# Kernel tuning notes

Hardware: AMD Instinct MI355X
Metric: run time of the kernel (lower is better)

The kernel has to match this reference:

```python
import jax, jax.numpy as jnp
import numpy as np

N_NODES = 100000
N_EDGES = 1600000
F_IN = 128
F_OUT = 32


def setup_inputs() -> dict:
    key = jax.random.key(0)
    k1, k2, k3 = jax.random.split(key, 3)
    x = jax.random.normal(k1, (N_NODES, F_IN), dtype=jnp.float32)
    edge_index = jax.random.randint(k2, (2, N_EDGES), 0, N_NODES, dtype=jnp.int64)
    # Glorot-style init for the GCNConv linear weight [F_IN, F_OUT]
    W = jax.random.normal(k3, (F_IN, F_OUT), dtype=jnp.float32) * (1.0 / np.sqrt(F_IN))
    b = jnp.zeros((F_OUT,), dtype=jnp.float32)
    return {"x": x, "edge_index": edge_index, "W": W, "b": b}


def reference(x, edge_index, W, b):
    N = x.shape[0]
    # --- add self loops (PyG GCNConv default) ---
    loops = jnp.arange(N, dtype=edge_index.dtype)
    src = jnp.concatenate([edge_index[0], loops])  # message sources j
    dst = jnp.concatenate([edge_index[1], loops])  # aggregation targets i
    # --- symmetric normalization: deg^-1/2[src] * deg^-1/2[dst] ---
    ones = jnp.ones(src.shape[0], dtype=x.dtype)
    deg = jax.ops.segment_sum(ones, dst, num_segments=N)  # in-degree incl. self loop
    dinv = jnp.where(deg > 0, jax.lax.rsqrt(deg), jnp.zeros_like(deg))
    norm = dinv[src] * dinv[dst]  # [E+N]
    # --- linear transform then gather-scale-scatter aggregate ---
    h = x @ W  # [N, F_OUT]
    msgs = h[src] * norm[:, None]  # [E+N, F_OUT]
    out = jax.ops.segment_sum(msgs, dst, num_segments=N)  # [N, F_OUT]
    return out + b
```

## Files before the change

kernel.cpp:

```cpp
#include <hip/hip_runtime.h>
#include <hip/hip_fp16.h>

#define N_NODES 100000
#define N_EDGES 1600000
#define F_IN    128
#define F_OUT   32

#define BKT_SHIFT  7
#define BKT_SIZE   128
#define NBKT       782
#define BKT_STRIDE 2560
#define BIN_TILE   4096
#define EPT        16
#define NTILES     ((N_EDGES + BIN_TILE - 1) / BIN_TILE)

#define AGG_SPLIT  4
#define SUB        32
#define SUB_STRIDE 768

typedef _Float16 f16x8 __attribute__((ext_vector_type(8)));
typedef float    f32x4 __attribute__((ext_vector_type(4)));

__global__ void init_kernel(int* __restrict__ gcur) {
    int i = blockIdx.x * blockDim.x + threadIdx.x;
    if (i < NBKT) gcur[i] = 0;
}

__global__ __launch_bounds__(256) void bin_kernel(const int* __restrict__ ei,
                                                  int* __restrict__ gcur,
                                                  unsigned int* __restrict__ binned) {
    __shared__ int cnt[NBKT], pos[NBKT], gbase[NBKT];
    int t = threadIdx.x;
    for (int b = t; b < NBKT; b += 256) { cnt[b] = 0; pos[b] = 0; }
    __syncthreads();
    int ebase = blockIdx.x * BIN_TILE;
    unsigned int pk[EPT];
    short bkt[EPT];
#pragma unroll
    for (int k = 0; k < EPT; ++k) {
        int e = ebase + k * 256 + t;
        if (e < N_EDGES) {
            int s = ei[e];
            int d = ei[N_EDGES + e];
            bkt[k] = (short)(d >> BKT_SHIFT);
            pk[k]  = (unsigned)s | ((unsigned)(d & (BKT_SIZE - 1)) << 25);
            atomicAdd(&cnt[bkt[k]], 1);
        } else {
            bkt[k] = -1;
        }
    }
    __syncthreads();
    for (int b = t; b < NBKT; b += 256)
        if (cnt[b] > 0) gbase[b] = atomicAdd(&gcur[b], cnt[b]);
    __syncthreads();
#pragma unroll
    for (int k = 0; k < EPT; ++k) {
        if (bkt[k] >= 0) {
            int r = atomicAdd(&pos[bkt[k]], 1);
            int p = gbase[bkt[k]] + r;
            if (p < BKT_STRIDE)
                binned[(size_t)bkt[k] * BKT_STRIDE + p] = pk[k];
        }
    }
}

__global__ __launch_bounds__(256) void dinv_from_bins_kernel(const unsigned int* __restrict__ binned,
                                                             const int* __restrict__ gcur,
                                                             float* __restrict__ dinv) {
    __shared__ int cnt[BKT_SIZE];
    int t = threadIdx.x;
    int b = blockIdx.x;
    if (t < BKT_SIZE) cnt[t] = 0;
    __syncthreads();
    int ne = gcur[b];
    if (ne > BKT_STRIDE) ne = BKT_STRIDE;
    const unsigned int* eb = binned + (size_t)b * BKT_STRIDE;
    for (int i = t; i < ne; i += 256)
        atomicAdd(&cnt[eb[i] >> 25], 1);
    __syncthreads();
    int gnode = b * BKT_SIZE + t;
    if (t < BKT_SIZE && gnode < N_NODES)
        dinv[gnode] = rsqrtf((float)(cnt[t] + 1));
}

#define WH_STRIDE 136
__global__ __launch_bounds__(256) void matmul_kernel(const float4* __restrict__ x4,
                                                     const float* __restrict__ W,
                                                     const float* __restrict__ dinv,
                                                     __half* __restrict__ hs) {
    __shared__ _Float16 Wh[F_OUT * WH_STRIDE];
    int t = threadIdx.x;
    {
        int col = t & 31, kb = (t >> 5) * 16;
        for (int u = 0; u < 16; ++u)
            Wh[col * WH_STRIDE + kb + u] = (_Float16)W[(kb + u) * F_OUT + col];
    }
    __syncthreads();

    int w = t >> 6, l = t & 63;
    int lr = l & 15, kg = l >> 4;
    int row = blockIdx.x * 64 + w * 16 + lr;
    const float4* xr = x4 + (size_t)row * 32;
    bool rok = row < N_NODES;

    f16x8 a[4];
#pragma unroll
    for (int ks = 0; ks < 4; ++ks) {
        float4 v0, v1;
        if (rok) {
            v0 = xr[ks * 8 + kg * 2];
            v1 = xr[ks * 8 + kg * 2 + 1];
        } else {
            v0 = make_float4(0, 0, 0, 0);
            v1 = v0;
        }
        f16x8 av;
        av[0] = (_Float16)v0.x; av[1] = (_Float16)v0.y;
        av[2] = (_Float16)v0.z; av[3] = (_Float16)v0.w;
        av[4] = (_Float16)v1.x; av[5] = (_Float16)v1.y;
        av[6] = (_Float16)v1.z; av[7] = (_Float16)v1.w;
        a[ks] = av;
    }

    f32x4 c0 = {0.f, 0.f, 0.f, 0.f}, c1 = {0.f, 0.f, 0.f, 0.f};
#pragma unroll
    for (int ks = 0; ks < 4; ++ks) {
        f16x8 b0 = *(const f16x8*)&Wh[lr * WH_STRIDE + ks * 32 + kg * 8];
        f16x8 b1 = *(const f16x8*)&Wh[(16 + lr) * WH_STRIDE + ks * 32 + kg * 8];
        c0 = __builtin_amdgcn_mfma_f32_16x16x32_f16(a[ks], b0, c0, 0, 0, 0);
        c1 = __builtin_amdgcn_mfma_f32_16x16x32_f16(a[ks], b1, c1, 0, 0, 0);
    }

    int orow0 = blockIdx.x * 64 + w * 16 + kg * 4;
#pragma unroll
    for (int i = 0; i < 4; ++i) {
        int orow = orow0 + i;
        if (orow < N_NODES) {
            float dv = dinv[orow];
            hs[(size_t)orow * F_OUT + lr]      = (__half)(c0[i] * dv);
            hs[(size_t)orow * F_OUT + 16 + lr] = (__half)(c1[i] * dv);
        }
    }
}

__device__ inline void acc4(uint2 u, float& a0, float& a1, float& a2, float& a3) {
    float2 f0 = __half22float2(*(__half2*)&u.x);
    float2 f1 = __half22float2(*(__half2*)&u.y);
    a0 += f0.x; a1 += f0.y; a2 += f1.x; a3 += f1.y;
}

__global__ __launch_bounds__(256) void aggregate_kernel(const unsigned int* __restrict__ binned,
                                                        const int* __restrict__ gcur,
                                                        const uint2* __restrict__ hs4,
                                                        const float* __restrict__ dinv,
                                                        const float* __restrict__ bias,
                                                        float* __restrict__ out) {
    __shared__ int scan[SUB];
    __shared__ int rp[SUB + 1];
    __shared__ int cur[SUB];
    __shared__ int se[SUB_STRIDE];
    int t = threadIdx.x;
    int b   = blockIdx.x >> 2;
    int sub = blockIdx.x & 3;
    int ne = gcur[b];
    if (ne > BKT_STRIDE) ne = BKT_STRIDE;
    const unsigned int* eb = binned + (size_t)b * BKT_STRIDE;

    if (t < SUB) scan[t] = 0;
    __syncthreads();

    unsigned pk[10];
#pragma unroll
    for (int k = 0; k < 10; ++k) {
        int i = t + k * 256;
        pk[k] = (i < ne) ? eb[i] : 0xFFFFFFFFu;
    }
#pragma unroll
    for (int k = 0; k < 10; ++k) {
        if (pk[k] != 0xFFFFFFFFu) {
            int dl = (int)(pk[k] >> 25);
            if ((dl >> 5) == sub) atomicAdd(&scan[dl & 31], 1);
        }
    }
    __syncthreads();
    int v = (t < SUB) ? scan[t] : 0;
    for (int off = 1; off < SUB; off <<= 1) {
        int add = (t < SUB && t >= off) ? scan[t - off] : 0;
        __syncthreads();
        if (t < SUB) scan[t] += add;
        __syncthreads();
    }
    if (t < SUB) {
        int ex = scan[t] - v;
        if (ex > SUB_STRIDE) ex = SUB_STRIDE;
        rp[t] = ex;
        cur[t] = ex;
    }
    if (t == 0) rp[SUB] = (scan[SUB - 1] < SUB_STRIDE) ? 0 : SUB_STRIDE;
    __syncthreads();
    if (t == 0) {
        int tot = scan[SUB - 1];
        rp[SUB] = (tot > SUB_STRIDE) ? SUB_STRIDE : tot;
    }
    __syncthreads();
#pragma unroll
    for (int k = 0; k < 10; ++k) {
        if (pk[k] != 0xFFFFFFFFu) {
            int dl = (int)(pk[k] >> 25);
            if ((dl >> 5) == sub) {
                int r = atomicAdd(&cur[dl & 31], 1);
                if (r < SUB_STRIDE) se[r] = (int)(pk[k] & 0x1FFFFFF);
            }
        }
    }
    __syncthreads();

    int n = t >> 3, j4 = t & 7;
    int gnode = b * BKT_SIZE + sub * SUB + n;
    if (gnode >= N_NODES) return;
    float4 bv = *(const float4*)&bias[j4 * 4];
    int beg = rp[n], end = rp[n + 1];
    float a0 = 0.f, a1 = 0.f, a2 = 0.f, a3 = 0.f;
    int p = beg;
    for (; p + 7 < end; p += 8) {
        uint2 u0 = hs4[(size_t)se[p]     * 8 + j4];
        uint2 u1 = hs4[(size_t)se[p + 1] * 8 + j4];
        uint2 u2 = hs4[(size_t)se[p + 2] * 8 + j4];
        uint2 u3 = hs4[(size_t)se[p + 3] * 8 + j4];
        uint2 u4 = hs4[(size_t)se[p + 4] * 8 + j4];
        uint2 u5 = hs4[(size_t)se[p + 5] * 8 + j4];
        uint2 u6 = hs4[(size_t)se[p + 6] * 8 + j4];
        uint2 u7 = hs4[(size_t)se[p + 7] * 8 + j4];
        acc4(u0, a0, a1, a2, a3); acc4(u1, a0, a1, a2, a3);
        acc4(u2, a0, a1, a2, a3); acc4(u3, a0, a1, a2, a3);
        acc4(u4, a0, a1, a2, a3); acc4(u5, a0, a1, a2, a3);
        acc4(u6, a0, a1, a2, a3); acc4(u7, a0, a1, a2, a3);
    }
    for (; p + 3 < end; p += 4) {
        uint2 u0 = hs4[(size_t)se[p]     * 8 + j4];
        uint2 u1 = hs4[(size_t)se[p + 1] * 8 + j4];
        uint2 u2 = hs4[(size_t)se[p + 2] * 8 + j4];
        uint2 u3 = hs4[(size_t)se[p + 3] * 8 + j4];
        acc4(u0, a0, a1, a2, a3); acc4(u1, a0, a1, a2, a3);
        acc4(u2, a0, a1, a2, a3); acc4(u3, a0, a1, a2, a3);
    }
    for (; p < end; ++p) {
        uint2 u0 = hs4[(size_t)se[p] * 8 + j4];
        acc4(u0, a0, a1, a2, a3);
    }
    float dv = dinv[gnode];
    uint2 us = hs4[(size_t)gnode * 8 + j4];
    float2 s0 = __half22float2(*(__half2*)&us.x);
    float2 s1 = __half22float2(*(__half2*)&us.y);
    float4 o;
    o.x = bv.x + dv * (a0 + s0.x);
    o.y = bv.y + dv * (a1 + s0.y);
    o.z = bv.z + dv * (a2 + s1.x);
    o.w = bv.w + dv * (a3 + s1.y);
    *(float4*)&out[(size_t)gnode * F_OUT + j4 * 4] = o;
}

extern "C" void kernel_launch(void* const* d_in, const int* in_sizes, int n_in,
                              void* d_out, int out_size, void* d_ws, size_t ws_size,
                              hipStream_t stream) {
    const float* x  = (const float*)d_in[0];
    const int*   ei = (const int*)d_in[1];
    const float* W  = (const float*)d_in[2];
    const float* b  = (const float*)d_in[3];
    float* out = (float*)d_out;

    int*          gcur   = (int*)d_ws;
    unsigned int* binned = (unsigned int*)(gcur + 1024);
    float*        dinv   = (float*)(binned + (size_t)NBKT * BKT_STRIDE);
    __half*       hs     = (__half*)(dinv + ((N_NODES + 3) & ~3));

    const int B = 256;

    init_kernel<<<1, 1024, 0, stream>>>(gcur);

    bin_kernel<<<NTILES, B, 0, stream>>>(ei, gcur, binned);

    dinv_from_bins_kernel<<<NBKT, B, 0, stream>>>(binned, gcur, dinv);

    matmul_kernel<<<(N_NODES + 63) / 64, B, 0, stream>>>((const float4*)x, W, dinv, hs);

    aggregate_kernel<<<NBKT * AGG_SPLIT, B, 0, stream>>>(binned, gcur, (const uint2*)hs, dinv, b, out);
}
```

Measured before the change: 75.13 us.

## Fuse degree computation into matmul and reuse atomic ranks in binning

Removes the separate dinv kernel. Each matmul block now covers one 128-node bucket, counts that bucket's in-degrees in shared memory and applies the normalization locally. The aggregate kernel computes dinv from its own per-node counts instead of reading a global array. Both bin and aggregate kernels keep the rank returned by the first shared atomic, which drops the second atomic pass. Binning uses 512-thread blocks with larger tiles. The cost is an extra pass over the binned edges inside matmul and larger blocks, which may lower occupancy.

```diff
diff --git a/kernel.cpp b/kernel.cpp
--- a/kernel.cpp
+++ b/kernel.cpp
@@ -10,9 +10,11 @@
 #define BKT_SIZE   128
 #define NBKT       782
 #define BKT_STRIDE 2560
-#define BIN_TILE   4096
-#define EPT        16
-#define NTILES     ((N_EDGES + BIN_TILE - 1) / BIN_TILE)
+
+#define BIN_THREADS 512
+#define BIN_TILE    8192
+#define EPT         (BIN_TILE / BIN_THREADS)
+#define NTILES      ((N_EDGES + BIN_TILE - 1) / BIN_TILE)
 
 #define AGG_SPLIT  4
 #define SUB        32
@@ -26,80 +28,76 @@
     if (i < NBKT) gcur[i] = 0;
 }
 
-__global__ __launch_bounds__(256) void bin_kernel(const int* __restrict__ ei,
-                                                  int* __restrict__ gcur,
-                                                  unsigned int* __restrict__ binned) {
-    __shared__ int cnt[NBKT], pos[NBKT], gbase[NBKT];
+__global__ __launch_bounds__(BIN_THREADS) void bin_kernel(const int* __restrict__ ei,
+                                                          int* __restrict__ gcur,
+                                                          unsigned int* __restrict__ binned) {
+    __shared__ int cnt[NBKT], gbase[NBKT];
     int t = threadIdx.x;
-    for (int b = t; b < NBKT; b += 256) { cnt[b] = 0; pos[b] = 0; }
+    for (int b = t; b < NBKT; b += BIN_THREADS) cnt[b] = 0;
     __syncthreads();
     int ebase = blockIdx.x * BIN_TILE;
     unsigned int pk[EPT];
+    int rk[EPT];
     short bkt[EPT];
 #pragma unroll
     for (int k = 0; k < EPT; ++k) {
-        int e = ebase + k * 256 + t;
+        int e = ebase + k * BIN_THREADS + t;
         if (e < N_EDGES) {
             int s = ei[e];
             int d = ei[N_EDGES + e];
             bkt[k] = (short)(d >> BKT_SHIFT);
             pk[k]  = (unsigned)s | ((unsigned)(d & (BKT_SIZE - 1)) << 25);
-            atomicAdd(&cnt[bkt[k]], 1);
+            rk[k]  = atomicAdd(&cnt[bkt[k]], 1);
         } else {
             bkt[k] = -1;
         }
     }
     __syncthreads();
-    for (int b = t; b < NBKT; b += 256)
+    for (int b = t; b < NBKT; b += BIN_THREADS)
         if (cnt[b] > 0) gbase[b] = atomicAdd(&gcur[b], cnt[b]);
     __syncthreads();
 #pragma unroll
     for (int k = 0; k < EPT; ++k) {
         if (bkt[k] >= 0) {
-            int r = atomicAdd(&pos[bkt[k]], 1);
-            int p = gbase[bkt[k]] + r;
+            int p = gbase[bkt[k]] + rk[k];
             if (p < BKT_STRIDE)
                 binned[(size_t)bkt[k] * BKT_STRIDE + p] = pk[k];
         }
     }
 }
 
-__global__ __launch_bounds__(256) void dinv_from_bins_kernel(const unsigned int* __restrict__ binned,
-                                                             const int* __restrict__ gcur,
-                                                             float* __restrict__ dinv) {
-    __shared__ int cnt[BKT_SIZE];
+#define WH_STRIDE 136
+__global__ __launch_bounds__(512) void matmul_kernel(const float4* __restrict__ x4,
+                                                     const float* __restrict__ W,
+                                                     const unsigned int* __restrict__ binned,
+                                                     const int* __restrict__ gcur,
+                                                     __half* __restrict__ hs) {
+    __shared__ _Float16 Wh[F_OUT * WH_STRIDE];
+    __shared__ int cnt128[BKT_SIZE];
+    __shared__ float dinvL[BKT_SIZE];
     int t = threadIdx.x;
     int b = blockIdx.x;
-    if (t < BKT_SIZE) cnt[t] = 0;
-    __syncthreads();
+
+    if (t < BKT_SIZE) cnt128[t] = 0;
+    {
+        int col = t & 31, kb = (t >> 5) * 8;
+        for (int u = 0; u < 8; ++u)
+            Wh[col * WH_STRIDE + kb + u] = (_Float16)W[(kb + u) * F_OUT + col];
+    }
+    __syncthreads();
+
     int ne = gcur[b];
     if (ne > BKT_STRIDE) ne = BKT_STRIDE;
     const unsigned int* eb = binned + (size_t)b * BKT_STRIDE;
-    for (int i = t; i < ne; i += 256)
-        atomicAdd(&cnt[eb[i] >> 25], 1);
-    __syncthreads();
-    int gnode = b * BKT_SIZE + t;
-    if (t < BKT_SIZE && gnode < N_NODES)
-        dinv[gnode] = rsqrtf((float)(cnt[t] + 1));
-}
-
-#define WH_STRIDE 136
-__global__ __launch_bounds__(256) void matmul_kernel(const float4* __restrict__ x4,
-                                                     const float* __restrict__ W,
-                                                     const float* __restrict__ dinv,
-                                                     __half* __restrict__ hs) {
-    __shared__ _Float16 Wh[F_OUT * WH_STRIDE];
-    int t = threadIdx.x;
-    {
-        int col = t & 31, kb = (t >> 5) * 16;
-        for (int u = 0; u < 16; ++u)
-            Wh[col * WH_STRIDE + kb + u] = (_Float16)W[(kb + u) * F_OUT + col];
-    }
+    for (int i = t; i < ne; i += 512)
+        atomicAdd(&cnt128[eb[i] >> 25], 1);
+    __syncthreads();
+    if (t < BKT_SIZE) dinvL[t] = rsqrtf((float)(cnt128[t] + 1));
     __syncthreads();
 
     int w = t >> 6, l = t & 63;
     int lr = l & 15, kg = l >> 4;
-    int row = blockIdx.x * 64 + w * 16 + lr;
+    int row = b * 128 + w * 16 + lr;
     const float4* xr = x4 + (size_t)row * 32;
     bool rok = row < N_NODES;
 
@@ -131,12 +129,12 @@
         c1 = __builtin_amdgcn_mfma_f32_16x16x32_f16(a[ks], b1, c1, 0, 0, 0);
     }
 
-    int orow0 = blockIdx.x * 64 + w * 16 + kg * 4;
+    int lrow0 = w * 16 + kg * 4;
 #pragma unroll
     for (int i = 0; i < 4; ++i) {
-        int orow = orow0 + i;
+        int orow = b * 128 + lrow0 + i;
         if (orow < N_NODES) {
-            float dv = dinv[orow];
+            float dv = dinvL[lrow0 + i];
             hs[(size_t)orow * F_OUT + lr]      = (__half)(c0[i] * dv);
             hs[(size_t)orow * F_OUT + 16 + lr] = (__half)(c1[i] * dv);
         }
@@ -152,12 +150,11 @@
 __global__ __launch_bounds__(256) void aggregate_kernel(const unsigned int* __restrict__ binned,
                                                         const int* __restrict__ gcur,
                                                         const uint2* __restrict__ hs4,
-                                                        const float* __restrict__ dinv,
                                                         const float* __restrict__ bias,
                                                         float* __restrict__ out) {
-    __shared__ int scan[SUB];
+    __shared__ int cnt[SUB];
+    __shared__ int sc[SUB];
     __shared__ int rp[SUB + 1];
-    __shared__ int cur[SUB];
     __shared__ int se[SUB_STRIDE];
     int t = threadIdx.x;
     int b   = blockIdx.x >> 2;
@@ -166,10 +163,11 @@
     if (ne > BKT_STRIDE) ne = BKT_STRIDE;
     const unsigned int* eb = binned + (size_t)b * BKT_STRIDE;
 
-    if (t < SUB) scan[t] = 0;
+    if (t < SUB) cnt[t] = 0;
     __syncthreads();
 
     unsigned pk[10];
+    int rk[10];
 #pragma unroll
     for (int k = 0; k < 10; ++k) {
         int i = t + k * 256;
@@ -177,40 +175,39 @@
     }
 #pragma unroll
     for (int k = 0; k < 10; ++k) {
+        rk[k] = -1;
         if (pk[k] != 0xFFFFFFFFu) {
             int dl = (int)(pk[k] >> 25);
-            if ((dl >> 5) == sub) atomicAdd(&scan[dl & 31], 1);
-        }
-    }
-    __syncthreads();
-    int v = (t < SUB) ? scan[t] : 0;
+            if ((dl >> 5) == sub) rk[k] = atomicAdd(&cnt[dl & 31], 1);
+        }
+    }
+    __syncthreads();
+    int v = (t < SUB) ? cnt[t] : 0;
+    if (t < SUB) sc[t] = v;
+    __syncthreads();
     for (int off = 1; off < SUB; off <<= 1) {
-        int add = (t < SUB && t >= off) ? scan[t - off] : 0;
+        int add = (t < SUB && t >= off) ? sc[t - off] : 0;
         __syncthreads();
-        if (t < SUB) scan[t] += add;
+        if (t < SUB) sc[t] += add;
         __syncthreads();
     }
     if (t < SUB) {
-        int ex = scan[t] - v;
-        if (ex > SUB_STRIDE) ex = SUB_STRIDE;
-        rp[t] = ex;
-        cur[t] = ex;
-    }
-    if (t == 0) rp[SUB] = (scan[SUB - 1] < SUB_STRIDE) ? 0 : SUB_STRIDE;
+        int ex = sc[t] - v;
+        rp[t] = (ex < SUB_STRIDE) ? ex : SUB_STRIDE;
+    }
+    if (t == 0) rp[SUB] = 0;
     __syncthreads();
     if (t == 0) {
-        int tot = scan[SUB - 1];
+        int tot = sc[SUB - 1];
         rp[SUB] = (tot > SUB_STRIDE) ? SUB_STRIDE : tot;
     }
     __syncthreads();
 #pragma unroll
     for (int k = 0; k < 10; ++k) {
-        if (pk[k] != 0xFFFFFFFFu) {
+        if (rk[k] >= 0) {
             int dl = (int)(pk[k] >> 25);
-            if ((dl >> 5) == sub) {
-                int r = atomicAdd(&cur[dl & 31], 1);
-                if (r < SUB_STRIDE) se[r] = (int)(pk[k] & 0x1FFFFFF);
-            }
+            int pos = rp[dl & 31] + rk[k];
+            if (pos < SUB_STRIDE) se[pos] = (int)(pk[k] & 0x1FFFFFF);
         }
     }
     __syncthreads();
@@ -219,7 +216,10 @@
     int gnode = b * BKT_SIZE + sub * SUB + n;
     if (gnode >= N_NODES) return;
     float4 bv = *(const float4*)&bias[j4 * 4];
-    int beg = rp[n], end = rp[n + 1];
+    int deg = cnt[n];
+    int beg = rp[n];
+    int end = rp[n + 1];
+    if (beg + deg < end) end = beg + deg;
     float a0 = 0.f, a1 = 0.f, a2 = 0.f, a3 = 0.f;
     int p = beg;
     for (; p + 7 < end; p += 8) {
@@ -248,7 +248,7 @@
         uint2 u0 = hs4[(size_t)se[p] * 8 + j4];
         acc4(u0, a0, a1, a2, a3);
     }
-    float dv = dinv[gnode];
+    float dv = rsqrtf((float)(deg + 1));
     uint2 us = hs4[(size_t)gnode * 8 + j4];
     float2 s0 = __half22float2(*(__half2*)&us.x);
     float2 s1 = __half22float2(*(__half2*)&us.y);
@@ -271,18 +271,13 @@
 
     int*          gcur   = (int*)d_ws;
     unsigned int* binned = (unsigned int*)(gcur + 1024);
-    float*        dinv   = (float*)(binned + (size_t)NBKT * BKT_STRIDE);
-    __half*       hs     = (__half*)(dinv + ((N_NODES + 3) & ~3));
-
-    const int B = 256;
+    __half*       hs     = (__half*)(binned + (size_t)NBKT * BKT_STRIDE);
 
     init_kernel<<<1, 1024, 0, stream>>>(gcur);
 
-    bin_kernel<<<NTILES, B, 0, stream>>>(ei, gcur, binned);
-
-    dinv_from_bins_kernel<<<NBKT, B, 0, stream>>>(binned, gcur, dinv);
-
-    matmul_kernel<<<(N_NODES + 63) / 64, B, 0, stream>>>((const float4*)x, W, dinv, hs);
-
-    aggregate_kernel<<<NBKT * AGG_SPLIT, B, 0, stream>>>(binned, gcur, (const uint2*)hs, dinv, b, out);
-}
+    bin_kernel<<<NTILES, BIN_THREADS, 0, stream>>>(ei, gcur, binned);
+
+    matmul_kernel<<<NBKT, 512, 0, stream>>>((const float4*)x, W, binned, gcur, hs);
+
+    aggregate_kernel<<<NBKT * AGG_SPLIT, 256, 0, stream>>>(binned, gcur, (const uint2*)hs, b, out);
+}
```

Measured after the change: 68.08 us. 1.1x faster.
